# Kernel tuning notes

Hardware: AMD Instinct MI355X
Metric: run time of the kernel (lower is better)

Reference implementation:

```python
import jax, jax.numpy as jnp
import numpy as np

B, N, DIN = 8, 50000, 16
E, M, CH = 800000, 25000, 64
C_HALF = CH // 2


def setup_inputs() -> dict:
    key = jax.random.key(0)
    ks = jax.random.split(key, 9)
    x = jax.random.normal(ks[0], (B, N, DIN), dtype=jnp.float32)
    adj_rows = jax.random.randint(ks[1], (E,), 0, N, dtype=jnp.int32)
    adj_cols = jax.random.randint(ks[2], (E,), 0, N, dtype=jnp.int32)
    adj_vals = jax.random.uniform(ks[3], (E,), dtype=jnp.float32)
    centroids = jax.random.randint(ks[4], (M,), 0, N, dtype=jnp.int32)
    # Conv1d(kernel_size=1) weights == dense [out, in] matrices
    W_lin = jax.random.normal(ks[5], (C_HALF, DIN), dtype=jnp.float32) * (1.0 / np.sqrt(DIN))
    b_lin = jax.random.normal(ks[6], (C_HALF,), dtype=jnp.float32) * 0.01
    W_eye = jax.random.normal(ks[7], (C_HALF, DIN), dtype=jnp.float32) * (1.0 / np.sqrt(DIN))
    b_eye = jax.random.normal(ks[8], (C_HALF,), dtype=jnp.float32) * 0.01
    return {"x": x, "adj_rows": adj_rows, "adj_cols": adj_cols, "adj_vals": adj_vals,
            "centroids": centroids, "W_lin": W_lin, "b_lin": b_lin,
            "W_eye": W_eye, "b_eye": b_eye}


def reference(x, adj_rows, adj_cols, adj_vals, centroids, W_lin, b_lin, W_eye, b_eye):
    # x: [B, N, DIN] -> permute to channels-first [B, DIN, N]
    xc = jnp.transpose(x, (0, 2, 1))
    # eye branch: 1x1 conv == pointwise linear over channel dim
    eye_x = jnp.einsum('bcn,oc->bon', xc, W_eye) + b_eye[None, :, None]  # [B, C/2, N]
    # SpMM aggregation: adj @ x.T where x is [B*DIN, N]
    xt = xc.reshape(-1, xc.shape[-1]).T                      # [N, B*DIN]
    msgs = adj_vals[:, None] * xt[adj_cols]                  # [E, B*DIN] gather
    agg = jax.ops.segment_sum(msgs, adj_rows, num_segments=xt.shape[0])  # [N, B*DIN] scatter-add
    xa = agg.T.reshape(xc.shape)                             # [B, DIN, N]
    lin_x = jnp.einsum('bcn,oc->bon', xa, W_lin) + b_lin[None, :, None]  # [B, C/2, N]
    out = jax.nn.relu(jnp.concatenate([lin_x, eye_x], axis=1))  # [B, C, N]
    out = out[:, :, centroids]                               # gather centroid nodes [B, C, M]
    return jnp.transpose(out, (0, 2, 1))                     # [B, M, C]
```

## Files before the change

kernel.cpp:

```cpp
#include <hip/hip_runtime.h>

#define DIN   16
#define BB    8
#define FDIM  128
#define CHALF 32
#define CH    64
#define CAP   52

__global__ void mark_kernel(const int* __restrict__ centroids, int* __restrict__ seen,
                            int* __restrict__ rankid, int* __restrict__ active_list,
                            int* __restrict__ nactive, int M) {
    int i = blockIdx.x * blockDim.x + threadIdx.x;
    if (i >= M) return;
    int n = centroids[i];
    if (atomicExch(&seen[n], 1) == 0) {
        int r = atomicAdd(nactive, 1);
        rankid[n] = r + 1;
        active_list[r] = n;
    }
}

__global__ void cr_kernel(const int* __restrict__ centroids, const int* __restrict__ rankid,
                          int* __restrict__ cr, int M) {
    int i = blockIdx.x * blockDim.x + threadIdx.x;
    if (i >= M) return;
    cr[i] = rankid[centroids[i]] - 1;
}

__global__ __launch_bounds__(256) void transpose_kernel(
    const float4* __restrict__ x4, float4* __restrict__ xt4, int N) {
    int t = blockIdx.x * 256 + threadIdx.x;
    int b = blockIdx.y;
    if (t >= N * 4) return;
    int n = t >> 2;
    int q = t & 3;
    xt4[(long long)n * 32 + b * 4 + q] = x4[(long long)b * N * 4 + t];
}

__global__ __launch_bounds__(256) void bin_kernel(
    const int* __restrict__ rows, const int* __restrict__ cols,
    const float* __restrict__ vals, const int* __restrict__ rankid,
    int* __restrict__ cnt, int2* __restrict__ bins, int E) {
    int e = blockIdx.x * blockDim.x + threadIdx.x;
    if (e >= E) return;
    int rr = rankid[rows[e]];
    if (rr == 0) return;
    int a = rr - 1;
    int pos = atomicAdd(&cnt[a], 1);
    if (pos < CAP)
        bins[(long long)a * CAP + pos] = make_int2(cols[e], __float_as_int(vals[e]));
}

__global__ __launch_bounds__(256) void gather_kernel(
    const float4* __restrict__ xt4, const int* __restrict__ cnt,
    const int2* __restrict__ bins, const int* __restrict__ active_list,
    const int* __restrict__ nactive,
    const float* __restrict__ W_lin, const float* __restrict__ b_lin,
    const float* __restrict__ W_eye, const float* __restrict__ b_eye,
    float* __restrict__ proj) {
    int tid = threadIdx.x;
    int w = tid >> 6;
    int l = tid & 63;

    __shared__ float sWc[DIN][CH + 1];
    __shared__ float sb[CH];
    __shared__ float sagg[4][FDIM];
    __shared__ float sx[4][FDIM];

    #pragma unroll
    for (int i = tid; i < CH * DIN; i += 256) {
        int o = i >> 4, cc = i & 15;
        sWc[cc][o] = (o < CHALF) ? W_lin[i] : W_eye[i - CHALF * DIN];
    }
    if (tid < CHALF) sb[tid] = b_lin[tid];
    else if (tid < CH) sb[tid] = b_eye[tid - CHALF];
    __syncthreads();

    int a = blockIdx.x * 4 + w;
    if (a >= *nactive) return;
    int n = active_list[a];
    int c = min(cnt[a], CAP);

    int g = l >> 5;
    int s = l & 31;

    int2 myedge = make_int2(0, 0);
    if (l < c) myedge = bins[(long long)a * CAP + l];
    float4 xrow = make_float4(0.f, 0.f, 0.f, 0.f);
    if (g == 0) xrow = xt4[(long long)n * 32 + s];

    int iters = (c + 1) >> 1;
    float4 acc = make_float4(0.f, 0.f, 0.f, 0.f);
    for (int i = 0; i < iters; ++i) {
        int k = 2 * i + g;
        int   col = __shfl(myedge.x, k);
        float v   = __int_as_float(__shfl(myedge.y, k));
        float4 sv = xt4[(long long)col * 32 + s];
        acc.x += v * sv.x; acc.y += v * sv.y; acc.z += v * sv.z; acc.w += v * sv.w;
    }
    acc.x += __shfl_xor(acc.x, 32);
    acc.y += __shfl_xor(acc.y, 32);
    acc.z += __shfl_xor(acc.z, 32);
    acc.w += __shfl_xor(acc.w, 32);
    if (g == 0) {
        ((float4*)sagg[w])[s] = acc;
        ((float4*)sx[w])[s]   = xrow;
    }

    int o = l;
    float wreg[DIN];
    #pragma unroll
    for (int cc = 0; cc < DIN; ++cc) wreg[cc] = sWc[cc][o];
    const float* src = (o < CHALF) ? sagg[w] : sx[w];
    float bias = sb[o];
    float* dst = proj + (long long)a * BB * CH + o;
    #pragma unroll
    for (int b = 0; b < BB; ++b) {
        float r = bias;
        #pragma unroll
        for (int cc = 0; cc < DIN; ++cc) r += wreg[cc] * src[b * DIN + cc];
        dst[(long long)b * CH] = fmaxf(r, 0.f);
    }
}

__global__ __launch_bounds__(256) void outcopy_kernel(
    const float4* __restrict__ proj4, const int* __restrict__ cr,
    float4* __restrict__ out4, int M) {
    int b = blockIdx.y;
    int t = blockIdx.x * 256 + threadIdx.x;
    int m = t >> 4;
    int l = t & 15;
    if (m >= M) return;
    int rk = cr[m];
    out4[((long long)b * M + m) * 16 + l] = proj4[((long long)rk * BB + b) * 16 + l];
}

extern "C" void kernel_launch(void* const* d_in, const int* in_sizes, int n_in,
                              void* d_out, int out_size, void* d_ws, size_t ws_size,
                              hipStream_t stream) {
    const float* x        = (const float*)d_in[0];
    const int*   adj_rows = (const int*)d_in[1];
    const int*   adj_cols = (const int*)d_in[2];
    const float* adj_vals = (const float*)d_in[3];
    const int*   cents    = (const int*)d_in[4];
    const float* W_lin    = (const float*)d_in[5];
    const float* b_lin    = (const float*)d_in[6];
    const float* W_eye    = (const float*)d_in[7];
    const float* b_eye    = (const float*)d_in[8];
    float* out = (float*)d_out;

    const int E = in_sizes[1];
    const int M = in_sizes[4];
    const int N = in_sizes[0] / (BB * DIN);

    char* p = (char*)d_ws;
    float* proj  = (float*)p;   p += (size_t)M * BB * CH * sizeof(float);
    float* xt    = (float*)p;   p += (size_t)N * FDIM * sizeof(float);
    int2*  bins  = (int2*)p;    p += (size_t)M * CAP * sizeof(int2);
    int*   cr    = (int*)p;     p += (size_t)M * sizeof(int);
    int*   alist = (int*)p;     p += (size_t)M * sizeof(int);
    char* zbase = p;
    int* seen    = (int*)p;     p += (size_t)N * sizeof(int);
    int* rankid  = (int*)p;     p += (size_t)N * sizeof(int);
    int* cnt     = (int*)p;     p += (size_t)M * sizeof(int);
    int* nactive = (int*)p;     p += 16 * sizeof(int);
    size_t zbytes = (size_t)(p - zbase);

    hipMemsetAsync(zbase, 0, zbytes, stream);

    dim3 tgrid((N * 4 + 255) / 256, BB);
    transpose_kernel<<<tgrid, 256, 0, stream>>>((const float4*)x, (float4*)xt, N);

    mark_kernel<<<(M + 255) / 256, 256, 0, stream>>>(cents, seen, rankid, alist, nactive, M);
    cr_kernel<<<(M + 255) / 256, 256, 0, stream>>>(cents, rankid, cr, M);
    bin_kernel<<<(E + 255) / 256, 256, 0, stream>>>(adj_rows, adj_cols, adj_vals,
                                                    rankid, cnt, bins, E);

    int gblocks = (M + 3) / 4;
    gather_kernel<<<gblocks, 256, 0, stream>>>((const float4*)xt, cnt, bins, alist, nactive,
                                               W_lin, b_lin, W_eye, b_eye, proj);

    dim3 ogrid((M * 16 + 255) / 256, BB);
    outcopy_kernel<<<ogrid, 256, 0, stream>>>((const float4*)proj, cr, (float4*)out, M);
}
```

Measured before the change: 182.0 us.

## Scatter projected rows directly to output via per-node centroid lists

Removes the intermediate proj buffer, the cr_kernel and the outcopy_kernel. mark_kernel now records, for each node, the list of centroid indices that map to it (capped at 16). gather_kernel writes its result straight to every output position for that node. This saves two launches and a full write-and-read pass over the intermediate, but the output writes become strided per lane (64 consecutive floats per batch) instead of float4 copies. It also adds an N*16 workspace list and cnt2 to the memset.

```diff
diff --git a/kernel.cpp b/kernel.cpp
--- a/kernel.cpp
+++ b/kernel.cpp
@@ -6,10 +6,12 @@
 #define CHALF 32
 #define CH    64
 #define CAP   52
+#define CAP2  16
 
 __global__ void mark_kernel(const int* __restrict__ centroids, int* __restrict__ seen,
                             int* __restrict__ rankid, int* __restrict__ active_list,
-                            int* __restrict__ nactive, int M) {
+                            int* __restrict__ nactive,
+                            int* __restrict__ cnt2, int* __restrict__ mlist, int M) {
     int i = blockIdx.x * blockDim.x + threadIdx.x;
     if (i >= M) return;
     int n = centroids[i];
@@ -18,13 +20,8 @@
         rankid[n] = r + 1;
         active_list[r] = n;
     }
-}
-
-__global__ void cr_kernel(const int* __restrict__ centroids, const int* __restrict__ rankid,
-                          int* __restrict__ cr, int M) {
-    int i = blockIdx.x * blockDim.x + threadIdx.x;
-    if (i >= M) return;
-    cr[i] = rankid[centroids[i]] - 1;
+    int pos = atomicAdd(&cnt2[n], 1);
+    if (pos < CAP2) mlist[n * CAP2 + pos] = i;
 }
 
 __global__ __launch_bounds__(256) void transpose_kernel(
@@ -55,9 +52,10 @@
     const float4* __restrict__ xt4, const int* __restrict__ cnt,
     const int2* __restrict__ bins, const int* __restrict__ active_list,
     const int* __restrict__ nactive,
+    const int* __restrict__ cnt2, const int* __restrict__ mlist,
     const float* __restrict__ W_lin, const float* __restrict__ b_lin,
     const float* __restrict__ W_eye, const float* __restrict__ b_eye,
-    float* __restrict__ proj) {
+    float* __restrict__ out, int M) {
     int tid = threadIdx.x;
     int w = tid >> 6;
     int l = tid & 63;
@@ -113,26 +111,23 @@
     for (int cc = 0; cc < DIN; ++cc) wreg[cc] = sWc[cc][o];
     const float* src = (o < CHALF) ? sagg[w] : sx[w];
     float bias = sb[o];
-    float* dst = proj + (long long)a * BB * CH + o;
+    float res[BB];
     #pragma unroll
     for (int b = 0; b < BB; ++b) {
         float r = bias;
         #pragma unroll
         for (int cc = 0; cc < DIN; ++cc) r += wreg[cc] * src[b * DIN + cc];
-        dst[(long long)b * CH] = fmaxf(r, 0.f);
+        res[b] = fmaxf(r, 0.f);
     }
-}
 
-__global__ __launch_bounds__(256) void outcopy_kernel(
-    const float4* __restrict__ proj4, const int* __restrict__ cr,
-    float4* __restrict__ out4, int M) {
-    int b = blockIdx.y;
-    int t = blockIdx.x * 256 + threadIdx.x;
-    int m = t >> 4;
-    int l = t & 15;
-    if (m >= M) return;
-    int rk = cr[m];
-    out4[((long long)b * M + m) * 16 + l] = proj4[((long long)rk * BB + b) * 16 + l];
+    int nm = min(cnt2[n], CAP2);
+    for (int mm = 0; mm < nm; ++mm) {
+        int m = mlist[n * CAP2 + mm];
+        float* dst = out + (long long)m * CH + o;
+        #pragma unroll
+        for (int b = 0; b < BB; ++b)
+            dst[(long long)b * M * CH] = res[b];
+    }
 }
 
 extern "C" void kernel_launch(void* const* d_in, const int* in_sizes, int n_in,
@@ -154,15 +149,15 @@
     const int N = in_sizes[0] / (BB * DIN);
 
     char* p = (char*)d_ws;
-    float* proj  = (float*)p;   p += (size_t)M * BB * CH * sizeof(float);
     float* xt    = (float*)p;   p += (size_t)N * FDIM * sizeof(float);
     int2*  bins  = (int2*)p;    p += (size_t)M * CAP * sizeof(int2);
-    int*   cr    = (int*)p;     p += (size_t)M * sizeof(int);
+    int*   mlist = (int*)p;     p += (size_t)N * CAP2 * sizeof(int);
     int*   alist = (int*)p;     p += (size_t)M * sizeof(int);
     char* zbase = p;
     int* seen    = (int*)p;     p += (size_t)N * sizeof(int);
     int* rankid  = (int*)p;     p += (size_t)N * sizeof(int);
     int* cnt     = (int*)p;     p += (size_t)M * sizeof(int);
+    int* cnt2    = (int*)p;     p += (size_t)N * sizeof(int);
     int* nactive = (int*)p;     p += 16 * sizeof(int);
     size_t zbytes = (size_t)(p - zbase);
 
@@ -171,15 +166,13 @@
     dim3 tgrid((N * 4 + 255) / 256, BB);
     transpose_kernel<<<tgrid, 256, 0, stream>>>((const float4*)x, (float4*)xt, N);
 
-    mark_kernel<<<(M + 255) / 256, 256, 0, stream>>>(cents, seen, rankid, alist, nactive, M);
-    cr_kernel<<<(M + 255) / 256, 256, 0, stream>>>(cents, rankid, cr, M);
+    mark_kernel<<<(M + 255) / 256, 256, 0, stream>>>(cents, seen, rankid, alist, nactive,
+                                                     cnt2, mlist, M);
     bin_kernel<<<(E + 255) / 256, 256, 0, stream>>>(adj_rows, adj_cols, adj_vals,
                                                     rankid, cnt, bins, E);
 
     int gblocks = (M + 3) / 4;
     gather_kernel<<<gblocks, 256, 0, stream>>>((const float4*)xt, cnt, bins, alist, nactive,
-                                               W_lin, b_lin, W_eye, b_eye, proj);
-
-    dim3 ogrid((M * 16 + 255) / 256, BB);
-    outcopy_kernel<<<ogrid, 256, 0, stream>>>((const float4*)proj, cr, (float4*)out, M);
+                                               cnt2, mlist,
+                                               W_lin, b_lin, W_eye, b_eye, out, M);
 }
```

Result: faster. 171.2 us (-5.9%).
